# Optimization experiments

Measured on AMD Instinct MI355X. Metric: run time of the kernel, lower is better.

## Reference

```python
import jax, jax.numpy as jnp
import numpy as np

D = 256
H = 8
HD = D // H
LN_EPS = 1e-5


def setup_inputs() -> dict:
    key = jax.random.key(0)
    ks = jax.random.split(key, 20)
    N = 768
    s = lambda *sh: 1.0 / np.sqrt(sh[-1])
    inp = {
        "features": jax.random.normal(ks[0], (N, D), jnp.float32),
        "boxes": jax.random.uniform(ks[1], (N, 4), jnp.float32),
        # MultiheadAttention params (torch layout: [out, in])
        "in_proj_w": jax.random.normal(ks[2], (3 * D, D), jnp.float32) * s(D),
        "in_proj_b": jnp.zeros((3 * D,), jnp.float32),
        "out_proj_w": jax.random.normal(ks[3], (D, D), jnp.float32) * s(D),
        "out_proj_b": jnp.zeros((D,), jnp.float32),
        # similarity_net params
        "w1": jax.random.normal(ks[4], (256, 3 * D + 3), jnp.float32) * s(3 * D + 3),
        "b1": jnp.zeros((256,), jnp.float32),
        "ln_g": jnp.ones((256,), jnp.float32),
        "ln_b": jnp.zeros((256,), jnp.float32),
        "w2": jax.random.normal(ks[5], (128, 256), jnp.float32) * s(256),
        "b2": jnp.zeros((128,), jnp.float32),
        "w3": jax.random.normal(ks[6], (64, 128), jnp.float32) * s(128),
        "b3": jnp.zeros((64,), jnp.float32),
        "w4": jax.random.normal(ks[7], (32, 64), jnp.float32) * s(64),
        "b4": jnp.zeros((32,), jnp.float32),
        "w5": jax.random.normal(ks[8], (1, 32), jnp.float32) * s(32),
        "b5": jnp.zeros((1,), jnp.float32),
    }
    return inp


def _mha(x, in_w, in_b, out_w, out_b):
    # x: [N, D]; torch nn.MultiheadAttention self-attention (eval mode)
    N = x.shape[0]
    qkv = x @ in_w.T + in_b                      # [N, 3D]
    q, k, v = jnp.split(qkv, 3, axis=-1)
    q = q.reshape(N, H, HD).transpose(1, 0, 2)   # [H, N, HD]
    k = k.reshape(N, H, HD).transpose(1, 0, 2)
    v = v.reshape(N, H, HD).transpose(1, 0, 2)
    scores = jnp.einsum("hnd,hmd->hnm", q, k) / np.sqrt(HD)
    attn = jax.nn.softmax(scores, axis=-1)
    o = jnp.einsum("hnm,hmd->hnd", attn, v)      # [H, N, HD]
    o = o.transpose(1, 0, 2).reshape(N, D)
    return o @ out_w.T + out_b


def reference(features, boxes, in_proj_w, in_proj_b, out_proj_w, out_proj_b,
              w1, b1, ln_g, ln_b, w2, b2, w3, b3, w4, b4, w5, b5):
    N = features.shape[0]
    att = _mha(features, in_proj_w, in_proj_b, out_proj_w, out_proj_b)  # [N, D]

    fi = jnp.broadcast_to(att[:, None, :], (N, N, D))
    fj = jnp.broadcast_to(att[None, :, :], (N, N, D))
    bi = boxes[:, None, :]
    bj = boxes[None, :, :]
    x_dist = jnp.abs(bi[:, :, 0] - bj[:, :, 0])
    y_diff = bi[:, :, 1] - bj[:, :, 1]
    spatial = jnp.stack([x_dist, jnp.abs(y_diff), y_diff], axis=-1)    # [N, N, 3]
    pairs = jnp.concatenate([fi, fj, fi * fj, spatial], axis=-1)       # [N, N, 3D+3]

    h = jax.nn.relu(pairs @ w1.T + b1)
    mu = jnp.mean(h, axis=-1, keepdims=True)
    var = jnp.var(h, axis=-1, keepdims=True)
    h = (h - mu) / jnp.sqrt(var + LN_EPS) * ln_g + ln_b
    h = jax.nn.relu(h @ w2.T + b2)
    h = jax.nn.relu(h @ w3.T + b3)
    h = jax.nn.relu(h @ w4.T + b4)
    logits = (h @ w5.T + b5)[..., 0]                                   # [N, N]

    eye = jnp.eye(N, dtype=logits.dtype)
    return logits * (1.0 - eye) - 1e9 * eye
```

## Files before the change

### kernel.cpp

```cpp
#include <hip/hip_runtime.h>


typedef __attribute__((ext_vector_type(8))) __bf16 bf16x8;
typedef __attribute__((ext_vector_type(4))) float f32x4;
typedef __attribute__((ext_vector_type(8))) int i32x8;

__device__ __forceinline__ float bf2f(unsigned short u) {
    return __uint_as_float(((unsigned int)u) << 16);
}
__device__ __forceinline__ unsigned short f2bf(float f) {
    union { __bf16 b; unsigned short u; } cv;
    cv.b = (__bf16)f;
    return cv.u;
}
__device__ __forceinline__ unsigned pk2(float lo, float hi) {
    return (unsigned)f2bf(lo) | ((unsigned)f2bf(hi) << 16);
}
__device__ __forceinline__ int pk4_fp8(float a, float b, float c, float d) {
    int w = __builtin_amdgcn_cvt_pk_fp8_f32(a, b, 0, false);
    w = __builtin_amdgcn_cvt_pk_fp8_f32(c, d, w, true);
    return w;
}
__device__ __forceinline__ unsigned char f2fp8(float v) {
    return (unsigned char)(__builtin_amdgcn_cvt_pk_fp8_f32(v, 0.f, 0, false) & 0xff);
}
__device__ __forceinline__ bf16x8 load8f_bf(const float* p) {
    float4 a = *reinterpret_cast<const float4*>(p);
    float4 b = *reinterpret_cast<const float4*>(p + 4);
    union { bf16x8 v; unsigned u[4]; } cv;
    cv.u[0] = pk2(a.x, a.y); cv.u[1] = pk2(a.z, a.w);
    cv.u[2] = pk2(b.x, b.y); cv.u[3] = pk2(b.z, b.w);
    return cv.v;
}
#define SC1 0x7F7F7F7F
#define MFMA_MX(a, b, c) __builtin_amdgcn_mfma_scale_f32_16x16x128_f8f6f4( \
        (a), (b), (c), 0, 0, 0, SC1, 0, SC1)

__global__ __launch_bounds__(256) void pack_all(
    const float* __restrict__ features, const float* __restrict__ in_proj_w,
    const float* __restrict__ in_proj_b, const float* __restrict__ out_proj_w,
    const float* __restrict__ w1, const float* __restrict__ w2,
    const float* __restrict__ w3, const float* __restrict__ w4,
    const float* __restrict__ b1, const float* __restrict__ ln_g,
    const float* __restrict__ ln_b, const float* __restrict__ b2,
    const float* __restrict__ out_proj_b,
    unsigned short* __restrict__ qkvb, unsigned short* __restrict__ Vt,
    unsigned short* __restrict__ WcatB,
    unsigned char* __restrict__ w1c_mx, unsigned char* __restrict__ w1t_f8,
    unsigned char* __restrict__ w2g_mx, unsigned char* __restrict__ w3_mx,
    unsigned char* __restrict__ w4_f8,
    float* __restrict__ bias768, float* __restrict__ c1, float* __restrict__ c2)
{
    const int blk = blockIdx.x;
    if (blk < 716) {
        int t = blk * 256 + threadIdx.x;
        if (t < 65536) {
            WcatB[t] = f2bf(out_proj_w[t]);
        } else if (t < 131072) {
            int u = t - 65536;
            int e = u & 31, lane = (u >> 5) & 63, f = u >> 11;
            int mt = f & 15, ks = f >> 4;
            int o = mt * 16 + (lane & 15);
            int k = ks * 128 + ((lane >> 4) & 3) * 32 + e;
            w1c_mx[u] = f2fp8(w1[o * 771 + 512 + k]);
        } else if (t < 139264) {
            int u = t - 131072;
            int e = u & 7, lane = (u >> 3) & 63, f = u >> 9;
            int o = f * 16 + (lane & 15);
            int k = ((lane >> 4) & 3) * 8 + e;
            float v = (k < 3) ? w1[o * 771 + 768 + k] : 0.f;
            w1t_f8[u] = f2fp8(v);
        } else if (t < 172032) {
            int u = t - 139264;
            int e = u & 31, lane = (u >> 5) & 63, f = u >> 11;
            int mt = f & 7, ks = f >> 3;
            int p = mt * 16 + (lane & 15);
            int k = ks * 128 + ((lane >> 4) & 3) * 32 + e;
            w2g_mx[u] = f2fp8(w2[p * 256 + k] * ln_g[k]);
        } else if (t < 180224) {
            int u = t - 172032;
            int e = u & 31, lane = (u >> 5) & 63, f = u >> 11;
            int o = f * 16 + (lane & 15);
            int k = ((lane >> 4) & 3) * 32 + e;
            w3_mx[u] = f2fp8(w3[o * 128 + k]);
        } else if (t < 182272) {
            int u = t - 180224;
            int e = u & 7, lane = (u >> 3) & 63, f = u >> 9;
            int l15 = lane & 15, quad = lane >> 4;
            int ct = f & 1, kc = f >> 1;
            int o = ct * 16 + l15, k = kc * 32 + quad * 8 + e;
            w4_f8[u] = f2fp8(w4[o * 64 + k]);
        } else if (t < 183040) {
            int n = t - 182272;
            if (n < 256) bias768[n] = out_proj_b[n];
            else {
                int m = n - 256;
                float s = 0.f;
                for (int d = 0; d < 256; d += 4) {
                    float4 ob = *reinterpret_cast<const float4*>(&out_proj_b[d]);
                    const float* wr = (m < 256) ? &w1[m * 771 + d]
                                                : &w1[(m - 256) * 771 + 256 + d];
                    float4 w = *reinterpret_cast<const float4*>(wr);
                    s += ob.x * w.x + ob.y * w.y + ob.z * w.z + ob.w * w.w;
                }
                bias768[n] = s + ((m < 256) ? b1[m] : 0.f);
            }
        } else if (t < 183168) {
            int p = t - 183040;
            float s2 = 0.f, s1 = 0.f;
            for (int k = 0; k < 256; k += 4) {
                float4 w = *reinterpret_cast<const float4*>(&w2[p * 256 + k]);
                float4 g = *reinterpret_cast<const float4*>(&ln_g[k]);
                float4 lb = *reinterpret_cast<const float4*>(&ln_b[k]);
                s2 += g.x * w.x + g.y * w.y + g.z * w.z + g.w * w.w;
                s1 += lb.x * w.x + lb.y * w.y + lb.z * w.z + lb.w * w.w;
            }
            c2[p] = s2;
            c1[p] = s1 + b2[p];
        }
    } else if (blk < 1228) {
        const int n = blk - 716, e = threadIdx.x;
        const float* wrow = (n < 256) ? &w1[n * 771] : &w1[(n - 256) * 771 + 256];
        float acc = 0.f;
        for (int d = 0; d < 256; d += 4) {
            float4 w = *reinterpret_cast<const float4*>(&wrow[d]);
            acc += w.x * out_proj_w[(d + 0) * 256 + e];
            acc += w.y * out_proj_w[(d + 1) * 256 + e];
            acc += w.z * out_proj_w[(d + 2) * 256 + e];
            acc += w.w * out_proj_w[(d + 3) * 256 + e];
        }
        WcatB[(256 + n) * 256 + e] = f2bf(acc);
    } else {
        const int q = blk - 1228;
        const int bm = q % 12, bn = q / 12;
        const int wv = threadIdx.x >> 6, lane = threadIdx.x & 63;
        const int l15 = lane & 15, quad = lane >> 4;
        const int row0 = bm * 64 + wv * 16;
        const int col0 = bn * 64;
        f32x4 acc[4] = {};
        for (int kc = 0; kc < 8; ++kc) {
            bf16x8 a = load8f_bf(&features[(row0 + l15) * 256 + kc * 32 + quad * 8]);
#pragma unroll
            for (int ct = 0; ct < 4; ++ct) {
                bf16x8 b = load8f_bf(&in_proj_w[(col0 + ct * 16 + l15) * 256 + kc * 32 + quad * 8]);
                acc[ct] = __builtin_amdgcn_mfma_f32_16x16x32_bf16(a, b, acc[ct], 0, 0, 0);
            }
        }
#pragma unroll
        for (int ct = 0; ct < 4; ++ct)
#pragma unroll
            for (int r = 0; r < 4; ++r) {
                int row = row0 + quad * 4 + r, col = col0 + ct * 16 + l15;
                float v = acc[ct][r] + in_proj_b[col];
                if (col < 512) qkvb[row * 768 + col] = f2bf(v);
                else           Vt[(col - 512) * 768 + row] = f2bf(v);
            }
    }
}

__global__ __launch_bounds__(256) void gemm_attab(
    const unsigned short* __restrict__ A, const unsigned short* __restrict__ W,
    const float* __restrict__ bias, float* __restrict__ att,
    float* __restrict__ AB)
{
    const int wv = threadIdx.x >> 6, lane = threadIdx.x & 63;
    const int l15 = lane & 15, quad = lane >> 4;
    const int row0 = blockIdx.x * 64 + wv * 16;
    const int col0 = blockIdx.y * 64;
    f32x4 acc[4] = {};
    for (int kc = 0; kc < 8; ++kc) {
        bf16x8 a = *reinterpret_cast<const bf16x8*>(&A[(row0 + l15) * 256 + kc * 32 + quad * 8]);
#pragma unroll
        for (int ct = 0; ct < 4; ++ct) {
            bf16x8 b = *reinterpret_cast<const bf16x8*>(&W[(col0 + ct * 16 + l15) * 256 + kc * 32 + quad * 8]);
            acc[ct] = __builtin_amdgcn_mfma_f32_16x16x32_bf16(a, b, acc[ct], 0, 0, 0);
        }
    }
#pragma unroll
    for (int ct = 0; ct < 4; ++ct)
#pragma unroll
        for (int r = 0; r < 4; ++r) {
            int row = row0 + quad * 4 + r, col = col0 + ct * 16 + l15;
            float v = acc[ct][r] + bias[col];
            if (col < 256) att[row * 256 + col] = v;
            else           AB[row * 512 + (col - 256)] = v;
        }
}

#define SP 776

__global__ __launch_bounds__(256) void attn_mfma(
    const unsigned short* __restrict__ qkvb, const unsigned short* __restrict__ Vt,
    unsigned short* __restrict__ Obf)
{
    __shared__ __align__(16) unsigned short smS[32 * SP];
    __shared__ float s_inv[32];
    const int h = blockIdx.x, q0 = blockIdx.y * 32, hb = h * 32;
    const int tid = threadIdx.x, wave = tid >> 6, lane = tid & 63;
    const int l15 = lane & 15, quad = lane >> 4;

    bf16x8 af[2];
#pragma unroll
    for (int mt = 0; mt < 2; ++mt)
        af[mt] = *reinterpret_cast<const bf16x8*>(&qkvb[(q0 + mt * 16 + l15) * 768 + hb + quad * 8]);
#pragma unroll
    for (int ct = 0; ct < 12; ++ct) {
        int n0 = wave * 192 + ct * 16;
        bf16x8 b = *reinterpret_cast<const bf16x8*>(&qkvb[(n0 + l15) * 768 + 256 + hb + quad * 8]);
#pragma unroll
        for (int mt = 0; mt < 2; ++mt) {
            f32x4 c = {};
            c = __builtin_amdgcn_mfma_f32_16x16x32_bf16(af[mt], b, c, 0, 0, 0);
#pragma unroll
            for (int r = 0; r < 4; ++r)
                smS[(mt * 16 + quad * 4 + r) * SP + n0 + l15] =
                    f2bf(c[r] * 0.17677669529663689f);
        }
    }
    __syncthreads();

    {
        const int row = tid >> 3, part = tid & 7;
        unsigned short* rp = &smS[row * SP + part * 96];
        float ls = 0.f;
#pragma unroll
        for (int c8 = 0; c8 < 12; ++c8) {
            uint4 v = *reinterpret_cast<const uint4*>(&rp[c8 * 8]);
            const unsigned short* pe = reinterpret_cast<const unsigned short*>(&v);
            unsigned short o8[8];
#pragma unroll
            for (int e = 0; e < 8; ++e) {
                float ev = __expf(bf2f(pe[e]));
                ls += ev;
                o8[e] = f2bf(ev);
            }
            *reinterpret_cast<uint4*>(&rp[c8 * 8]) = *reinterpret_cast<const uint4*>(o8);
        }
        ls += __shfl_xor(ls, 1, 64);
        ls += __shfl_xor(ls, 2, 64);
        ls += __shfl_xor(ls, 4, 64);
        if (part == 0) s_inv[row] = 1.0f / ls;
    }
    __syncthreads();

    const int row0 = (wave >> 1) * 16, cg = wave & 1;
    f32x4 accp = {};
    for (int kc = 0; kc < 24; ++kc) {
        bf16x8 a = *reinterpret_cast<const bf16x8*>(&smS[(row0 + l15) * SP + kc * 32 + quad * 8]);
        bf16x8 b = *reinterpret_cast<const bf16x8*>(&Vt[(hb + cg * 16 + l15) * 768 + kc * 32 + quad * 8]);
        accp = __builtin_amdgcn_mfma_f32_16x16x32_bf16(a, b, accp, 0, 0, 0);
    }
#pragma unroll
    for (int r = 0; r < 4; ++r) {
        int rloc = row0 + quad * 4 + r;
        Obf[(q0 + rloc) * 256 + hb + cg * 16 + l15] = f2bf(accp[r] * s_inv[rloc]);
    }
}

__global__ __launch_bounds__(512, 2) void pair_mlp(
    const float* __restrict__ att, const float* __restrict__ AB,
    const unsigned char* __restrict__ w1c_mx, const unsigned char* __restrict__ w1t_f8,
    const unsigned char* __restrict__ w2g_mx, const unsigned char* __restrict__ w3_mx,
    const unsigned char* __restrict__ w4_f8,
    const float* __restrict__ boxes,
    const float* __restrict__ c1, const float* __restrict__ c2,
    const float* __restrict__ b3, const float* __restrict__ b4,
    const float* __restrict__ w5, const float* __restrict__ b5,
    float* __restrict__ out)
{
    __shared__ __align__(16) unsigned char smH[64 * 384];
    __shared__ __align__(16) unsigned char smH1[64 * 256];
    __shared__ __align__(16) unsigned char smH2[64 * 192];
    __shared__ __align__(16) unsigned char smH3[64 * 72];
    __shared__ float s_psum[64][8], s_pssq[64][8];
    __shared__ float s_mu[64], s_rs[64];
    __shared__ float s_l5[64][2];

    const int i    = blockIdx.x;
    const int j0   = blockIdx.y * 64;
    const int tid  = threadIdx.x;
    const int wave = tid >> 6;
    const int lane = tid & 63;
    const int l15  = lane & 15;
    const int quad = lane >> 4;

    {
        const int g = tid & 63;
        const int ch = g >> 2;
        float4 fi4 = *reinterpret_cast<const float4*>(&att[i * 256 + g * 4]);
#pragma unroll 4
        for (int it = 0; it < 8; ++it) {
            int r = (tid >> 6) + it * 8;
            float4 aj = *reinterpret_cast<const float4*>(&att[(j0 + r) * 256 + g * 4]);
            int cs = ch ^ (r & 15);
            *reinterpret_cast<int*>(&smH[r * 384 + cs * 16 + (g & 3) * 4]) =
                pk4_fp8(aj.x * fi4.x, aj.y * fi4.y, aj.z * fi4.z, aj.w * fi4.w);
        }
    }
    if (tid < 64) {
        int j = j0 + tid;
        float xd = fabsf(boxes[i * 4 + 0] - boxes[j * 4 + 0]);
        float yd = boxes[i * 4 + 1] - boxes[j * 4 + 1];
        unsigned char* tb = &smH[tid * 384 + 256 + (tid & 3) * 24];
        *reinterpret_cast<int*>(tb)      = pk4_fp8(xd, fabsf(yd), yd, 0.f);
        *reinterpret_cast<int*>(tb + 4)  = 0;
        *reinterpret_cast<long long*>(tb + 8)  = 0;
        *reinterpret_cast<long long*>(tb + 16) = 0;
        *reinterpret_cast<long long*>(tb + 24) = 0;
    }
    __syncthreads();

    f32x4 acc1[2][4] = {};
#pragma unroll
    for (int ks = 0; ks < 2; ++ks) {
        i32x8 a0 = *reinterpret_cast<const i32x8*>(&w1c_mx[((ks * 16 + wave * 2 + 0) * 64 + lane) * 32]);
        i32x8 a1 = *reinterpret_cast<const i32x8*>(&w1c_mx[((ks * 16 + wave * 2 + 1) * 64 + lane) * 32]);
        const int cb = ks * 8 + quad * 2;
#pragma unroll
        for (int nt = 0; nt < 4; ++nt) {
            const unsigned char* rp = &smH[(nt * 16 + l15) * 384];
            union { i32x8 v; uint4 q[2]; } b;
            b.q[0] = *reinterpret_cast<const uint4*>(rp + ((cb    ) ^ l15) * 16);
            b.q[1] = *reinterpret_cast<const uint4*>(rp + ((cb + 1) ^ l15) * 16);
            acc1[0][nt] = MFMA_MX(a0, b.v, acc1[0][nt]);
            acc1[1][nt] = MFMA_MX(a1, b.v, acc1[1][nt]);
        }
    }
    {
        long long a0 = *reinterpret_cast<const long long*>(&w1t_f8[((wave * 2 + 0) * 64 + lane) * 8]);
        long long a1 = *reinterpret_cast<const long long*>(&w1t_f8[((wave * 2 + 1) * 64 + lane) * 8]);
#pragma unroll
        for (int nt = 0; nt < 4; ++nt) {
            long long b = *reinterpret_cast<const long long*>(
                &smH[(nt * 16 + l15) * 384 + 256 + (l15 & 3) * 24 + quad * 8]);
            acc1[0][nt] = __builtin_amdgcn_mfma_f32_16x16x32_fp8_fp8(a0, b, acc1[0][nt], 0, 0, 0);
            acc1[1][nt] = __builtin_amdgcn_mfma_f32_16x16x32_fp8_fp8(a1, b, acc1[1][nt], 0, 0, 0);
        }
    }

    const int o0 = wave * 32;
    float vsum[4] = {}, vssq[4] = {};
#pragma unroll
    for (int mt = 0; mt < 2; ++mt) {
        int o = o0 + mt * 16 + quad * 4;
        float4 Ai = *reinterpret_cast<const float4*>(&AB[i * 512 + o]);
        float AiA[4] = {Ai.x, Ai.y, Ai.z, Ai.w};
#pragma unroll
        for (int nt = 0; nt < 4; ++nt) {
            int j = nt * 16 + l15;
            float4 Bj = *reinterpret_cast<const float4*>(&AB[(j0 + j) * 512 + 256 + o]);
            float BjA[4] = {Bj.x, Bj.y, Bj.z, Bj.w};
#pragma unroll
            for (int r = 0; r < 4; ++r) {
                float v = fmaxf(acc1[mt][nt][r] + AiA[r] + BjA[r], 0.f);
                acc1[mt][nt][r] = v;
                vsum[nt] += v; vssq[nt] += v * v;
            }
        }
    }
#pragma unroll
    for (int nt = 0; nt < 4; ++nt) {
        vsum[nt] += __shfl_xor(vsum[nt], 16, 64);
        vsum[nt] += __shfl_xor(vsum[nt], 32, 64);
        vssq[nt] += __shfl_xor(vssq[nt], 16, 64);
        vssq[nt] += __shfl_xor(vssq[nt], 32, 64);
    }
    if (quad == 0)
#pragma unroll
        for (int nt = 0; nt < 4; ++nt) {
            s_psum[nt * 16 + l15][wave] = vsum[nt];
            s_pssq[nt * 16 + l15][wave] = vssq[nt];
        }
#pragma unroll
    for (int mt = 0; mt < 2; ++mt) {
        const int ch = wave * 2 + mt;
#pragma unroll
        for (int nt = 0; nt < 4; ++nt) {
            int j = nt * 16 + l15;
            *reinterpret_cast<int*>(&smH1[j * 256 + (ch ^ l15) * 16 + quad * 4]) =
                pk4_fp8(acc1[mt][nt][0], acc1[mt][nt][1], acc1[mt][nt][2], acc1[mt][nt][3]);
        }
    }
    __syncthreads();
    if (wave == 0) {
        int j = lane;
        float sm = 0.f, sq = 0.f;
#pragma unroll
        for (int w = 0; w < 8; ++w) { sm += s_psum[j][w]; sq += s_pssq[j][w]; }
        sm *= (1.0f / 256.0f); sq *= (1.0f / 256.0f);
        s_mu[j] = sm;
        s_rs[j] = rsqrtf(sq - sm * sm + 1e-5f);
    }

    f32x4 acc2[4] = {};
#pragma unroll
    for (int ks = 0; ks < 2; ++ks) {
        i32x8 a = *reinterpret_cast<const i32x8*>(&w2g_mx[((ks * 8 + wave) * 64 + lane) * 32]);
        const int cb = ks * 8 + quad * 2;
#pragma unroll
        for (int nt = 0; nt < 4; ++nt) {
            const unsigned char* rp = &smH1[(nt * 16 + l15) * 256];
            union { i32x8 v; uint4 q[2]; } b;
            b.q[0] = *reinterpret_cast<const uint4*>(rp + ((cb    ) ^ l15) * 16);
            b.q[1] = *reinterpret_cast<const uint4*>(rp + ((cb + 1) ^ l15) * 16);
            acc2[nt] = MFMA_MX(a, b.v, acc2[nt]);
        }
    }
    __syncthreads();
    {
        int p = wave * 16 + quad * 4;
        float4 C1 = *reinterpret_cast<const float4*>(&c1[p]);
        float4 C2 = *reinterpret_cast<const float4*>(&c2[p]);
        float C1A[4] = {C1.x, C1.y, C1.z, C1.w};
        float C2A[4] = {C2.x, C2.y, C2.z, C2.w};
#pragma unroll
        for (int nt = 0; nt < 4; ++nt) {
            int j = nt * 16 + l15;
            float mu = s_mu[j], rs = s_rs[j];
            float vv[4];
#pragma unroll
            for (int r = 0; r < 4; ++r)
                vv[r] = fmaxf(rs * (acc2[nt][r] - mu * C2A[r]) + C1A[r], 0.f);
            *reinterpret_cast<int*>(&smH2[j * 192 + (wave ^ (l15 & 7)) * 16 + quad * 4]) =
                pk4_fp8(vv[0], vv[1], vv[2], vv[3]);
        }
    }
    __syncthreads();

    const int qt  = wave >> 1;
    const int jh2 = wave & 1;
    f32x4 acc3[2] = {};
    {
        i32x8 a = *reinterpret_cast<const i32x8*>(&w3_mx[(qt * 64 + lane) * 32]);
        const int cb = quad * 2;
#pragma unroll
        for (int ntl = 0; ntl < 2; ++ntl) {
            int j = (jh2 * 2 + ntl) * 16 + l15;
            const unsigned char* rp = &smH2[j * 192];
            union { i32x8 v; uint4 q[2]; } b;
            b.q[0] = *reinterpret_cast<const uint4*>(rp + ((cb    ) ^ (l15 & 7)) * 16);
            b.q[1] = *reinterpret_cast<const uint4*>(rp + ((cb + 1) ^ (l15 & 7)) * 16);
            acc3[ntl] = MFMA_MX(a, b.v, acc3[ntl]);
        }
    }
    {
        int q = qt * 16 + quad * 4;
        float4 B3 = *reinterpret_cast<const float4*>(&b3[q]);
        float B3A[4] = {B3.x, B3.y, B3.z, B3.w};
#pragma unroll
        for (int ntl = 0; ntl < 2; ++ntl) {
            int j = (jh2 * 2 + ntl) * 16 + l15;
            float vv[4];
#pragma unroll
            for (int r = 0; r < 4; ++r)
                vv[r] = fmaxf(acc3[ntl][r] + B3A[r], 0.f);
            *reinterpret_cast<int*>(&smH3[j * 72 + q]) = pk4_fp8(vv[0], vv[1], vv[2], vv[3]);
        }
    }
    __syncthreads();

    const int mt4 = wave & 1;
    const int jq  = wave >> 1;
    f32x4 acc4 = {};
#pragma unroll
    for (int kc = 0; kc < 2; ++kc) {
        long long a = *reinterpret_cast<const long long*>(&w4_f8[((kc * 2 + mt4) * 64 + lane) * 8]);
        int j = jq * 16 + l15;
        long long b = *reinterpret_cast<const long long*>(&smH3[j * 72 + kc * 32 + quad * 8]);
        acc4 = __builtin_amdgcn_mfma_f32_16x16x32_fp8_fp8(a, b, acc4, 0, 0, 0);
    }
    {
        int o4 = mt4 * 16 + quad * 4;
        float4 B4 = *reinterpret_cast<const float4*>(&b4[o4]);
        float4 W5 = *reinterpret_cast<const float4*>(&w5[o4]);
        float B4A[4] = {B4.x, B4.y, B4.z, B4.w};
        float W5A[4] = {W5.x, W5.y, W5.z, W5.w};
        float part = 0.f;
#pragma unroll
        for (int r = 0; r < 4; ++r)
            part += fmaxf(acc4[r] + B4A[r], 0.f) * W5A[r];
        part += __shfl_xor(part, 16, 64);
        part += __shfl_xor(part, 32, 64);
        if (quad == 0)
            s_l5[jq * 16 + l15][mt4] = part;
    }
    __syncthreads();
    if (tid < 64) {
        int j = j0 + tid;
        float v = s_l5[tid][0] + s_l5[tid][1] + b5[0];
        out[i * 768 + j] = (j == i) ? -1.0e9f : v;
    }
}

extern "C" void kernel_launch(void* const* d_in, const int* in_sizes, int n_in,
                              void* d_out, int out_size, void* d_ws, size_t ws_size,
                              hipStream_t stream)
{
    const float* features   = (const float*)d_in[0];
    const float* boxes      = (const float*)d_in[1];
    const float* in_proj_w  = (const float*)d_in[2];
    const float* in_proj_b  = (const float*)d_in[3];
    const float* out_proj_w = (const float*)d_in[4];
    const float* out_proj_b = (const float*)d_in[5];
    const float* w1  = (const float*)d_in[6];
    const float* b1  = (const float*)d_in[7];
    const float* ln_g = (const float*)d_in[8];
    const float* ln_b = (const float*)d_in[9];
    const float* w2  = (const float*)d_in[10];
    const float* b2  = (const float*)d_in[11];
    const float* w3  = (const float*)d_in[12];
    const float* b3  = (const float*)d_in[13];
    const float* w4  = (const float*)d_in[14];
    const float* b4  = (const float*)d_in[15];
    const float* w5  = (const float*)d_in[16];
    const float* b5  = (const float*)d_in[17];
    float* out = (float*)d_out;

    char* p = (char*)d_ws;
    unsigned short* qkvb  = (unsigned short*)p; p += 768 * 768 * 2;
    unsigned short* Vt    = (unsigned short*)p; p += 256 * 768 * 2;
    unsigned short* Obf   = (unsigned short*)p; p += 768 * 256 * 2;
    unsigned short* WcatB = (unsigned short*)p; p += 196608 * 2;
    float* att = (float*)p; p += 768 * 256 * 4;
    float* AB  = (float*)p; p += 768 * 512 * 4;
    unsigned char* w1c_mx = (unsigned char*)p; p += 65536;
    unsigned char* w1t_f8 = (unsigned char*)p; p += 8192;
    unsigned char* w2g_mx = (unsigned char*)p; p += 32768;
    unsigned char* w3_mx  = (unsigned char*)p; p += 8192;
    unsigned char* w4_f8  = (unsigned char*)p; p += 2048;
    float* bias768 = (float*)p; p += 768 * 4;
    float* c1v     = (float*)p; p += 128 * 4;
    float* c2v     = (float*)p; p += 128 * 4;

    pack_all<<<dim3(1372), dim3(256), 0, stream>>>(features, in_proj_w,
        in_proj_b, out_proj_w, w1, w2, w3, w4, b1, ln_g, ln_b, b2, out_proj_b,
        qkvb, Vt, WcatB, w1c_mx, w1t_f8, w2g_mx, w3_mx, w4_f8,
        bias768, c1v, c2v);
    attn_mfma<<<dim3(8, 24), dim3(256), 0, stream>>>(qkvb, Vt, Obf);
    gemm_attab<<<dim3(12, 12), dim3(256), 0, stream>>>(Obf, WcatB, bias768,
        att, AB);
    pair_mlp<<<dim3(768, 12), dim3(512), 0, stream>>>(att, AB,
        w1c_mx, w1t_f8, w2g_mx, w3_mx, w4_f8, boxes, c1v, c2v,
        b3, b4, w5, b5, out);
}
```

Measured before the change: 283.1 us.

## Process two 64-column tiles per block with software-pipelined MLP stages

The pair MLP kernel now handles 128 j-columns per block as two 64-wide tiles, interleaving the layer stages of tile A with those of tile B in a reused shared-memory pool, so that independent GEMMs sit between barriers. The layer-norm statistics are now accumulated with shared-memory atomics instead of per-wave partials plus a reduction pass, and the padded tile row stride shrinks from 384 to 352 bytes. This halves the grid, amortises the fi row load and weight-fragment reloads, and aims to hide latency. The costs are more register pressure and fewer blocks, which may reduce occupancy or tail balance.

```diff
diff --git a/kernel.cpp b/kernel.cpp
--- a/kernel.cpp
+++ b/kernel.cpp
@@ -257,6 +257,238 @@
     }
 }
 
+#define STRA 352
+
+__device__ __forceinline__ void stage_tile(
+    const float* __restrict__ att, const float* __restrict__ boxes,
+    int i, int j0, unsigned char* dst, int tid)
+{
+    const int g = tid & 63;
+    const int ch = g >> 2;
+    float4 fi4 = *reinterpret_cast<const float4*>(&att[i * 256 + g * 4]);
+#pragma unroll 4
+    for (int it = 0; it < 8; ++it) {
+        int r = (tid >> 6) + it * 8;
+        float4 aj = *reinterpret_cast<const float4*>(&att[(j0 + r) * 256 + g * 4]);
+        int cs = ch ^ (r & 15);
+        *reinterpret_cast<int*>(&dst[r * STRA + cs * 16 + (g & 3) * 4]) =
+            pk4_fp8(aj.x * fi4.x, aj.y * fi4.y, aj.z * fi4.z, aj.w * fi4.w);
+    }
+    if (tid < 64) {
+        int j = j0 + tid;
+        float xd = fabsf(boxes[i * 4 + 0] - boxes[j * 4 + 0]);
+        float yd = boxes[i * 4 + 1] - boxes[j * 4 + 1];
+        unsigned char* tb = &dst[tid * STRA + 256 + (tid & 3) * 16];
+        *reinterpret_cast<int*>(tb)      = pk4_fp8(xd, fabsf(yd), yd, 0.f);
+        *reinterpret_cast<int*>(tb + 4)  = 0;
+        *reinterpret_cast<long long*>(tb + 8)  = 0;
+        *reinterpret_cast<long long*>(tb + 16) = 0;
+        *reinterpret_cast<long long*>(tb + 24) = 0;
+    }
+}
+
+__device__ __forceinline__ void gemm1_t(
+    const unsigned char* __restrict__ w1c_mx, const unsigned char* __restrict__ w1t_f8,
+    const unsigned char* smH, f32x4 acc1[2][4], int wave, int lane, int l15, int quad)
+{
+#pragma unroll
+    for (int mt = 0; mt < 2; ++mt)
+#pragma unroll
+        for (int nt = 0; nt < 4; ++nt) acc1[mt][nt] = (f32x4){0.f, 0.f, 0.f, 0.f};
+#pragma unroll
+    for (int ks = 0; ks < 2; ++ks) {
+        i32x8 a0 = *reinterpret_cast<const i32x8*>(&w1c_mx[((ks * 16 + wave * 2 + 0) * 64 + lane) * 32]);
+        i32x8 a1 = *reinterpret_cast<const i32x8*>(&w1c_mx[((ks * 16 + wave * 2 + 1) * 64 + lane) * 32]);
+        const int cb = ks * 8 + quad * 2;
+#pragma unroll
+        for (int nt = 0; nt < 4; ++nt) {
+            const unsigned char* rp = &smH[(nt * 16 + l15) * STRA];
+            union { i32x8 v; uint4 q[2]; } b;
+            b.q[0] = *reinterpret_cast<const uint4*>(rp + ((cb    ) ^ l15) * 16);
+            b.q[1] = *reinterpret_cast<const uint4*>(rp + ((cb + 1) ^ l15) * 16);
+            acc1[0][nt] = MFMA_MX(a0, b.v, acc1[0][nt]);
+            acc1[1][nt] = MFMA_MX(a1, b.v, acc1[1][nt]);
+        }
+    }
+    {
+        long long a0 = *reinterpret_cast<const long long*>(&w1t_f8[((wave * 2 + 0) * 64 + lane) * 8]);
+        long long a1 = *reinterpret_cast<const long long*>(&w1t_f8[((wave * 2 + 1) * 64 + lane) * 8]);
+#pragma unroll
+        for (int nt = 0; nt < 4; ++nt) {
+            long long b = *reinterpret_cast<const long long*>(
+                &smH[(nt * 16 + l15) * STRA + 256 + (l15 & 3) * 16 + quad * 8]);
+            acc1[0][nt] = __builtin_amdgcn_mfma_f32_16x16x32_fp8_fp8(a0, b, acc1[0][nt], 0, 0, 0);
+            acc1[1][nt] = __builtin_amdgcn_mfma_f32_16x16x32_fp8_fp8(a1, b, acc1[1][nt], 0, 0, 0);
+        }
+    }
+}
+
+__device__ __forceinline__ void epi1_t(
+    const float* __restrict__ AB, int i, int j0, f32x4 acc1[2][4],
+    float* ssum, float* sssq, unsigned char* h1dst,
+    int wave, int l15, int quad)
+{
+    const int o0 = wave * 32;
+    float vsum[4] = {}, vssq[4] = {};
+#pragma unroll
+    for (int mt = 0; mt < 2; ++mt) {
+        int o = o0 + mt * 16 + quad * 4;
+        float4 Ai = *reinterpret_cast<const float4*>(&AB[i * 512 + o]);
+        float AiA[4] = {Ai.x, Ai.y, Ai.z, Ai.w};
+#pragma unroll
+        for (int nt = 0; nt < 4; ++nt) {
+            int j = nt * 16 + l15;
+            float4 Bj = *reinterpret_cast<const float4*>(&AB[(j0 + j) * 512 + 256 + o]);
+            float BjA[4] = {Bj.x, Bj.y, Bj.z, Bj.w};
+#pragma unroll
+            for (int r = 0; r < 4; ++r) {
+                float v = fmaxf(acc1[mt][nt][r] + AiA[r] + BjA[r], 0.f);
+                acc1[mt][nt][r] = v;
+                vsum[nt] += v; vssq[nt] += v * v;
+            }
+        }
+    }
+#pragma unroll
+    for (int nt = 0; nt < 4; ++nt) {
+        vsum[nt] += __shfl_xor(vsum[nt], 16, 64);
+        vsum[nt] += __shfl_xor(vsum[nt], 32, 64);
+        vssq[nt] += __shfl_xor(vssq[nt], 16, 64);
+        vssq[nt] += __shfl_xor(vssq[nt], 32, 64);
+    }
+    if (quad == 0)
+#pragma unroll
+        for (int nt = 0; nt < 4; ++nt) {
+            atomicAdd(&ssum[nt * 16 + l15], vsum[nt]);
+            atomicAdd(&sssq[nt * 16 + l15], vssq[nt]);
+        }
+#pragma unroll
+    for (int mt = 0; mt < 2; ++mt) {
+        const int ch = wave * 2 + mt;
+#pragma unroll
+        for (int nt = 0; nt < 4; ++nt) {
+            int j = nt * 16 + l15;
+            *reinterpret_cast<int*>(&h1dst[j * 256 + (ch ^ l15) * 16 + quad * 4]) =
+                pk4_fp8(acc1[mt][nt][0], acc1[mt][nt][1], acc1[mt][nt][2], acc1[mt][nt][3]);
+        }
+    }
+}
+
+__device__ __forceinline__ void gemm2_t(
+    const unsigned char* __restrict__ w2g_mx, const unsigned char* h1src,
+    f32x4 acc2[4], int wave, int lane, int l15, int quad)
+{
+#pragma unroll
+    for (int nt = 0; nt < 4; ++nt) acc2[nt] = (f32x4){0.f, 0.f, 0.f, 0.f};
+#pragma unroll
+    for (int ks = 0; ks < 2; ++ks) {
+        i32x8 a = *reinterpret_cast<const i32x8*>(&w2g_mx[((ks * 8 + wave) * 64 + lane) * 32]);
+        const int cb = ks * 8 + quad * 2;
+#pragma unroll
+        for (int nt = 0; nt < 4; ++nt) {
+            const unsigned char* rp = &h1src[(nt * 16 + l15) * 256];
+            union { i32x8 v; uint4 q[2]; } b;
+            b.q[0] = *reinterpret_cast<const uint4*>(rp + ((cb    ) ^ l15) * 16);
+            b.q[1] = *reinterpret_cast<const uint4*>(rp + ((cb + 1) ^ l15) * 16);
+            acc2[nt] = MFMA_MX(a, b.v, acc2[nt]);
+        }
+    }
+}
+
+__device__ __forceinline__ void epi2_t(
+    const float* __restrict__ c1, const float* __restrict__ c2,
+    const float* ssum, const float* sssq, f32x4 acc2[4], unsigned char* h2dst,
+    int wave, int l15, int quad)
+{
+    int p = wave * 16 + quad * 4;
+    float4 C1 = *reinterpret_cast<const float4*>(&c1[p]);
+    float4 C2 = *reinterpret_cast<const float4*>(&c2[p]);
+    float C1A[4] = {C1.x, C1.y, C1.z, C1.w};
+    float C2A[4] = {C2.x, C2.y, C2.z, C2.w};
+#pragma unroll
+    for (int nt = 0; nt < 4; ++nt) {
+        int j = nt * 16 + l15;
+        float mu = ssum[j] * (1.0f / 256.0f);
+        float rs = rsqrtf(sssq[j] * (1.0f / 256.0f) - mu * mu + 1e-5f);
+        float vv[4];
+#pragma unroll
+        for (int r = 0; r < 4; ++r)
+            vv[r] = fmaxf(rs * (acc2[nt][r] - mu * C2A[r]) + C1A[r], 0.f);
+        *reinterpret_cast<int*>(&h2dst[j * 192 + (wave ^ (l15 & 7)) * 16 + quad * 4]) =
+            pk4_fp8(vv[0], vv[1], vv[2], vv[3]);
+    }
+}
+
+__device__ __forceinline__ void gemm3_t(
+    const unsigned char* __restrict__ w3_mx, const unsigned char* h2src,
+    f32x4 acc3[2], int wave, int lane, int l15, int quad)
+{
+    const int qt  = wave >> 1;
+    const int jh2 = wave & 1;
+    acc3[0] = (f32x4){0.f, 0.f, 0.f, 0.f};
+    acc3[1] = (f32x4){0.f, 0.f, 0.f, 0.f};
+    i32x8 a = *reinterpret_cast<const i32x8*>(&w3_mx[(qt * 64 + lane) * 32]);
+    const int cb = quad * 2;
+#pragma unroll
+    for (int ntl = 0; ntl < 2; ++ntl) {
+        int j = (jh2 * 2 + ntl) * 16 + l15;
+        const unsigned char* rp = &h2src[j * 192];
+        union { i32x8 v; uint4 q[2]; } b;
+        b.q[0] = *reinterpret_cast<const uint4*>(rp + ((cb    ) ^ (l15 & 7)) * 16);
+        b.q[1] = *reinterpret_cast<const uint4*>(rp + ((cb + 1) ^ (l15 & 7)) * 16);
+        acc3[ntl] = MFMA_MX(a, b.v, acc3[ntl]);
+    }
+}
+
+__device__ __forceinline__ void epi3_t(
+    const float* __restrict__ b3, f32x4 acc3[2], unsigned char* h3dst,
+    int wave, int l15, int quad)
+{
+    const int qt  = wave >> 1;
+    const int jh2 = wave & 1;
+    int q = qt * 16 + quad * 4;
+    float4 B3 = *reinterpret_cast<const float4*>(&b3[q]);
+    float B3A[4] = {B3.x, B3.y, B3.z, B3.w};
+#pragma unroll
+    for (int ntl = 0; ntl < 2; ++ntl) {
+        int j = (jh2 * 2 + ntl) * 16 + l15;
+        float vv[4];
+#pragma unroll
+        for (int r = 0; r < 4; ++r)
+            vv[r] = fmaxf(acc3[ntl][r] + B3A[r], 0.f);
+        *reinterpret_cast<int*>(&h3dst[j * 72 + q]) = pk4_fp8(vv[0], vv[1], vv[2], vv[3]);
+    }
+}
+
+__device__ __forceinline__ void gemm4_head_t(
+    const unsigned char* __restrict__ w4_f8, const unsigned char* h3src,
+    const float* __restrict__ b4, const float* __restrict__ w5,
+    float (*l5)[2], int wave, int lane, int l15, int quad)
+{
+    const int mt4 = wave & 1;
+    const int jq  = wave >> 1;
+    f32x4 acc4 = {};
+#pragma unroll
+    for (int kc = 0; kc < 2; ++kc) {
+        long long a = *reinterpret_cast<const long long*>(&w4_f8[((kc * 2 + mt4) * 64 + lane) * 8]);
+        int j = jq * 16 + l15;
+        long long b = *reinterpret_cast<const long long*>(&h3src[j * 72 + kc * 32 + quad * 8]);
+        acc4 = __builtin_amdgcn_mfma_f32_16x16x32_fp8_fp8(a, b, acc4, 0, 0, 0);
+    }
+    int o4 = mt4 * 16 + quad * 4;
+    float4 B4 = *reinterpret_cast<const float4*>(&b4[o4]);
+    float4 W5 = *reinterpret_cast<const float4*>(&w5[o4]);
+    float B4A[4] = {B4.x, B4.y, B4.z, B4.w};
+    float W5A[4] = {W5.x, W5.y, W5.z, W5.w};
+    float part = 0.f;
+#pragma unroll
+    for (int r = 0; r < 4; ++r)
+        part += fmaxf(acc4[r] + B4A[r], 0.f) * W5A[r];
+    part += __shfl_xor(part, 16, 64);
+    part += __shfl_xor(part, 32, 64);
+    if (quad == 0)
+        l5[jq * 16 + l15][mt4] = part;
+}
+
 __global__ __launch_bounds__(512, 2) void pair_mlp(
     const float* __restrict__ att, const float* __restrict__ AB,
     const unsigned char* __restrict__ w1c_mx, const unsigned char* __restrict__ w1t_f8,
@@ -268,226 +500,66 @@
     const float* __restrict__ w5, const float* __restrict__ b5,
     float* __restrict__ out)
 {
-    __shared__ __align__(16) unsigned char smH[64 * 384];
-    __shared__ __align__(16) unsigned char smH1[64 * 256];
-    __shared__ __align__(16) unsigned char smH2[64 * 192];
-    __shared__ __align__(16) unsigned char smH3[64 * 72];
-    __shared__ float s_psum[64][8], s_pssq[64][8];
-    __shared__ float s_mu[64], s_rs[64];
-    __shared__ float s_l5[64][2];
+    __shared__ __align__(16) unsigned char smPool[22528 * 2 + 16384];
+    __shared__ float s_sum[2][64], s_ssq[2][64];
+    __shared__ float s_l5[2][64][2];
+
+    unsigned char* const R0 = smPool;
+    unsigned char* const R1 = smPool + 22528;
+    unsigned char* const R2 = smPool + 45056;
 
     const int i    = blockIdx.x;
-    const int j0   = blockIdx.y * 64;
+    const int j0A  = blockIdx.y * 128;
+    const int j0B  = j0A + 64;
     const int tid  = threadIdx.x;
     const int wave = tid >> 6;
     const int lane = tid & 63;
     const int l15  = lane & 15;
     const int quad = lane >> 4;
 
-    {
-        const int g = tid & 63;
-        const int ch = g >> 2;
-        float4 fi4 = *reinterpret_cast<const float4*>(&att[i * 256 + g * 4]);
-#pragma unroll 4
-        for (int it = 0; it < 8; ++it) {
-            int r = (tid >> 6) + it * 8;
-            float4 aj = *reinterpret_cast<const float4*>(&att[(j0 + r) * 256 + g * 4]);
-            int cs = ch ^ (r & 15);
-            *reinterpret_cast<int*>(&smH[r * 384 + cs * 16 + (g & 3) * 4]) =
-                pk4_fp8(aj.x * fi4.x, aj.y * fi4.y, aj.z * fi4.z, aj.w * fi4.w);
-        }
-    }
+    stage_tile(att, boxes, i, j0A, R0, tid);
+    if (tid < 128) { s_sum[tid >> 6][tid & 63] = 0.f; s_ssq[tid >> 6][tid & 63] = 0.f; }
+    __syncthreads();
+
+    f32x4 acc1[2][4];
+    gemm1_t(w1c_mx, w1t_f8, R0, acc1, wave, lane, l15, quad);
+    epi1_t(AB, i, j0A, acc1, s_sum[0], s_ssq[0], R2, wave, l15, quad);
+    stage_tile(att, boxes, i, j0B, R1, tid);
+    __syncthreads();
+
+    f32x4 acc2A[4];
+    gemm2_t(w2g_mx, R2, acc2A, wave, lane, l15, quad);
+    gemm1_t(w1c_mx, w1t_f8, R1, acc1, wave, lane, l15, quad);
+    epi1_t(AB, i, j0B, acc1, s_sum[1], s_ssq[1], R0, wave, l15, quad);
+    __syncthreads();
+
+    f32x4 acc2B[4];
+    gemm2_t(w2g_mx, R0, acc2B, wave, lane, l15, quad);
+    epi2_t(c1, c2, s_sum[0], s_ssq[0], acc2A, R2, wave, l15, quad);
+    __syncthreads();
+
+    f32x4 acc3[2];
+    gemm3_t(w3_mx, R2, acc3, wave, lane, l15, quad);
+    epi2_t(c1, c2, s_sum[1], s_ssq[1], acc2B, R1, wave, l15, quad);
+    epi3_t(b3, acc3, R0, wave, l15, quad);
+    __syncthreads();
+
+    gemm4_head_t(w4_f8, R0, b4, w5, s_l5[0], wave, lane, l15, quad);
+    gemm3_t(w3_mx, R1, acc3, wave, lane, l15, quad);
+    epi3_t(b3, acc3, R0 + 8192, wave, l15, quad);
+    __syncthreads();
+
     if (tid < 64) {
-        int j = j0 + tid;
-        float xd = fabsf(boxes[i * 4 + 0] - boxes[j * 4 + 0]);
-        float yd = boxes[i * 4 + 1] - boxes[j * 4 + 1];
-        unsigned char* tb = &smH[tid * 384 + 256 + (tid & 3) * 24];
-        *reinterpret_cast<int*>(tb)      = pk4_fp8(xd, fabsf(yd), yd, 0.f);
-        *reinterpret_cast<int*>(tb + 4)  = 0;
-        *reinterpret_cast<long long*>(tb + 8)  = 0;
-        *reinterpret_cast<long long*>(tb + 16) = 0;
-        *reinterpret_cast<long long*>(tb + 24) = 0;
-    }
-    __syncthreads();
-
-    f32x4 acc1[2][4] = {};
-#pragma unroll
-    for (int ks = 0; ks < 2; ++ks) {
-        i32x8 a0 = *reinterpret_cast<const i32x8*>(&w1c_mx[((ks * 16 + wave * 2 + 0) * 64 + lane) * 32]);
-        i32x8 a1 = *reinterpret_cast<const i32x8*>(&w1c_mx[((ks * 16 + wave * 2 + 1) * 64 + lane) * 32]);
-        const int cb = ks * 8 + quad * 2;
-#pragma unroll
-        for (int nt = 0; nt < 4; ++nt) {
-            const unsigned char* rp = &smH[(nt * 16 + l15) * 384];
-            union { i32x8 v; uint4 q[2]; } b;
-            b.q[0] = *reinterpret_cast<const uint4*>(rp + ((cb    ) ^ l15) * 16);
-            b.q[1] = *reinterpret_cast<const uint4*>(rp + ((cb + 1) ^ l15) * 16);
-            acc1[0][nt] = MFMA_MX(a0, b.v, acc1[0][nt]);
-            acc1[1][nt] = MFMA_MX(a1, b.v, acc1[1][nt]);
-        }
-    }
-    {
-        long long a0 = *reinterpret_cast<const long long*>(&w1t_f8[((wave * 2 + 0) * 64 + lane) * 8]);
-        long long a1 = *reinterpret_cast<const long long*>(&w1t_f8[((wave * 2 + 1) * 64 + lane) * 8]);
-#pragma unroll
-        for (int nt = 0; nt < 4; ++nt) {
-            long long b = *reinterpret_cast<const long long*>(
-                &smH[(nt * 16 + l15) * 384 + 256 + (l15 & 3) * 24 + quad * 8]);
-            acc1[0][nt] = __builtin_amdgcn_mfma_f32_16x16x32_fp8_fp8(a0, b, acc1[0][nt], 0, 0, 0);
-            acc1[1][nt] = __builtin_amdgcn_mfma_f32_16x16x32_fp8_fp8(a1, b, acc1[1][nt], 0, 0, 0);
-        }
-    }
-
-    const int o0 = wave * 32;
-    float vsum[4] = {}, vssq[4] = {};
-#pragma unroll
-    for (int mt = 0; mt < 2; ++mt) {
-        int o = o0 + mt * 16 + quad * 4;
-        float4 Ai = *reinterpret_cast<const float4*>(&AB[i * 512 + o]);
-        float AiA[4] = {Ai.x, Ai.y, Ai.z, Ai.w};
-#pragma unroll
-        for (int nt = 0; nt < 4; ++nt) {
-            int j = nt * 16 + l15;
-            float4 Bj = *reinterpret_cast<const float4*>(&AB[(j0 + j) * 512 + 256 + o]);
-            float BjA[4] = {Bj.x, Bj.y, Bj.z, Bj.w};
-#pragma unroll
-            for (int r = 0; r < 4; ++r) {
-                float v = fmaxf(acc1[mt][nt][r] + AiA[r] + BjA[r], 0.f);
-                acc1[mt][nt][r] = v;
-                vsum[nt] += v; vssq[nt] += v * v;
-            }
-        }
-    }
-#pragma unroll
-    for (int nt = 0; nt < 4; ++nt) {
-        vsum[nt] += __shfl_xor(vsum[nt], 16, 64);
-        vsum[nt] += __shfl_xor(vsum[nt], 32, 64);
-        vssq[nt] += __shfl_xor(vssq[nt], 16, 64);
-        vssq[nt] += __shfl_xor(vssq[nt], 32, 64);
-    }
-    if (quad == 0)
-#pragma unroll
-        for (int nt = 0; nt < 4; ++nt) {
-            s_psum[nt * 16 + l15][wave] = vsum[nt];
-            s_pssq[nt * 16 + l15][wave] = vssq[nt];
-        }
-#pragma unroll
-    for (int mt = 0; mt < 2; ++mt) {
-        const int ch = wave * 2 + mt;
-#pragma unroll
-        for (int nt = 0; nt < 4; ++nt) {
-            int j = nt * 16 + l15;
-            *reinterpret_cast<int*>(&smH1[j * 256 + (ch ^ l15) * 16 + quad * 4]) =
-                pk4_fp8(acc1[mt][nt][0], acc1[mt][nt][1], acc1[mt][nt][2], acc1[mt][nt][3]);
-        }
-    }
-    __syncthreads();
-    if (wave == 0) {
-        int j = lane;
-        float sm = 0.f, sq = 0.f;
-#pragma unroll
-        for (int w = 0; w < 8; ++w) { sm += s_psum[j][w]; sq += s_pssq[j][w]; }
-        sm *= (1.0f / 256.0f); sq *= (1.0f / 256.0f);
-        s_mu[j] = sm;
-        s_rs[j] = rsqrtf(sq - sm * sm + 1e-5f);
-    }
-
-    f32x4 acc2[4] = {};
-#pragma unroll
-    for (int ks = 0; ks < 2; ++ks) {
-        i32x8 a = *reinterpret_cast<const i32x8*>(&w2g_mx[((ks * 8 + wave) * 64 + lane) * 32]);
-        const int cb = ks * 8 + quad * 2;
-#pragma unroll
-        for (int nt = 0; nt < 4; ++nt) {
-            const unsigned char* rp = &smH1[(nt * 16 + l15) * 256];
-            union { i32x8 v; uint4 q[2]; } b;
-            b.q[0] = *reinterpret_cast<const uint4*>(rp + ((cb    ) ^ l15) * 16);
-            b.q[1] = *reinterpret_cast<const uint4*>(rp + ((cb + 1) ^ l15) * 16);
-            acc2[nt] = MFMA_MX(a, b.v, acc2[nt]);
-        }
-    }
-    __syncthreads();
-    {
-        int p = wave * 16 + quad * 4;
-        float4 C1 = *reinterpret_cast<const float4*>(&c1[p]);
-        float4 C2 = *reinterpret_cast<const float4*>(&c2[p]);
-        float C1A[4] = {C1.x, C1.y, C1.z, C1.w};
-        float C2A[4] = {C2.x, C2.y, C2.z, C2.w};
-#pragma unroll
-        for (int nt = 0; nt < 4; ++nt) {
-            int j = nt * 16 + l15;
-            float mu = s_mu[j], rs = s_rs[j];
-            float vv[4];
-#pragma unroll
-            for (int r = 0; r < 4; ++r)
-                vv[r] = fmaxf(rs * (acc2[nt][r] - mu * C2A[r]) + C1A[r], 0.f);
-            *reinterpret_cast<int*>(&smH2[j * 192 + (wave ^ (l15 & 7)) * 16 + quad * 4]) =
-                pk4_fp8(vv[0], vv[1], vv[2], vv[3]);
-        }
-    }
-    __syncthreads();
-
-    const int qt  = wave >> 1;
-    const int jh2 = wave & 1;
-    f32x4 acc3[2] = {};
-    {
-        i32x8 a = *reinterpret_cast<const i32x8*>(&w3_mx[(qt * 64 + lane) * 32]);
-        const int cb = quad * 2;
-#pragma unroll
-        for (int ntl = 0; ntl < 2; ++ntl) {
-            int j = (jh2 * 2 + ntl) * 16 + l15;
-            const unsigned char* rp = &smH2[j * 192];
-            union { i32x8 v; uint4 q[2]; } b;
-            b.q[0] = *reinterpret_cast<const uint4*>(rp + ((cb    ) ^ (l15 & 7)) * 16);
-            b.q[1] = *reinterpret_cast<const uint4*>(rp + ((cb + 1) ^ (l15 & 7)) * 16);
-            acc3[ntl] = MFMA_MX(a, b.v, acc3[ntl]);
-        }
-    }
-    {
-        int q = qt * 16 + quad * 4;
-        float4 B3 = *reinterpret_cast<const float4*>(&b3[q]);
-        float B3A[4] = {B3.x, B3.y, B3.z, B3.w};
-#pragma unroll
-        for (int ntl = 0; ntl < 2; ++ntl) {
-            int j = (jh2 * 2 + ntl) * 16 + l15;
-            float vv[4];
-#pragma unroll
-            for (int r = 0; r < 4; ++r)
-                vv[r] = fmaxf(acc3[ntl][r] + B3A[r], 0.f);
-            *reinterpret_cast<int*>(&smH3[j * 72 + q]) = pk4_fp8(vv[0], vv[1], vv[2], vv[3]);
-        }
-    }
-    __syncthreads();
-
-    const int mt4 = wave & 1;
-    const int jq  = wave >> 1;
-    f32x4 acc4 = {};
-#pragma unroll
-    for (int kc = 0; kc < 2; ++kc) {
-        long long a = *reinterpret_cast<const long long*>(&w4_f8[((kc * 2 + mt4) * 64 + lane) * 8]);
-        int j = jq * 16 + l15;
-        long long b = *reinterpret_cast<const long long*>(&smH3[j * 72 + kc * 32 + quad * 8]);
-        acc4 = __builtin_amdgcn_mfma_f32_16x16x32_fp8_fp8(a, b, acc4, 0, 0, 0);
-    }
-    {
-        int o4 = mt4 * 16 + quad * 4;
-        float4 B4 = *reinterpret_cast<const float4*>(&b4[o4]);
-        float4 W5 = *reinterpret_cast<const float4*>(&w5[o4]);
-        float B4A[4] = {B4.x, B4.y, B4.z, B4.w};
-        float W5A[4] = {W5.x, W5.y, W5.z, W5.w};
-        float part = 0.f;
-#pragma unroll
-        for (int r = 0; r < 4; ++r)
-            part += fmaxf(acc4[r] + B4A[r], 0.f) * W5A[r];
-        part += __shfl_xor(part, 16, 64);
-        part += __shfl_xor(part, 32, 64);
-        if (quad == 0)
-            s_l5[jq * 16 + l15][mt4] = part;
-    }
-    __syncthreads();
+        int j = j0A + tid;
+        float v = s_l5[0][tid][0] + s_l5[0][tid][1] + b5[0];
+        out[i * 768 + j] = (j == i) ? -1.0e9f : v;
+    }
+    gemm4_head_t(w4_f8, R0 + 8192, b4, w5, s_l5[1], wave, lane, l15, quad);
+    __syncthreads();
+
     if (tid < 64) {
-        int j = j0 + tid;
-        float v = s_l5[tid][0] + s_l5[tid][1] + b5[0];
+        int j = j0B + tid;
+        float v = s_l5[1][tid][0] + s_l5[1][tid][1] + b5[0];
         out[i * 768 + j] = (j == i) ? -1.0e9f : v;
     }
 }
@@ -539,7 +611,7 @@
     attn_mfma<<<dim3(8, 24), dim3(256), 0, stream>>>(qkvb, Vt, Obf);
     gemm_attab<<<dim3(12, 12), dim3(256), 0, stream>>>(Obf, WcatB, bias768,
         att, AB);
-    pair_mlp<<<dim3(768, 12), dim3(512), 0, stream>>>(att, AB,
+    pair_mlp<<<dim3(768, 6), dim3(512), 0, stream>>>(att, AB,
         w1c_mx, w1t_f8, w2g_mx, w3_mx, w4_f8, boxes, c1v, c2v,
         b3, b4, w5, b5, out);
 }
```

New measurement: 369.3 us. +30.4%, slower.
